# Kernel tuning notes

Hardware: AMD Instinct MI355X
Metric: run time of the kernel (lower is better)

The kernel has to match this reference:

```python
import jax, jax.numpy as jnp
import numpy as np

B, S, D = 4, 2048, 256
H, RANK, DFF = 8, 8, 1024
DK = D // H
EPS = 1e-5


def _linear(x, W, b):
    # torch nn.Linear: y = x @ W.T + b, W shape (out, in)
    return jnp.einsum('bsd,od->bso', x, W) + b


def _layer_norm(x, g, b):
    mu = jnp.mean(x, axis=-1, keepdims=True)
    var = jnp.var(x, axis=-1, keepdims=True)
    return (x - mu) * jax.lax.rsqrt(var + EPS) * g + b


def setup_inputs() -> dict:
    key = jax.random.key(0)
    ks = jax.random.split(key, 20)
    r = RANK * H
    s = lambda fan_in: 1.0 / np.sqrt(fan_in)
    inp = {
        'x': jax.random.normal(ks[0], (B, S, D), jnp.float32),
        'Wq_down': jax.random.uniform(ks[1], (r, D), jnp.float32, -s(D), s(D)),
        'bq_down': jnp.zeros((r,), jnp.float32),
        'Wq_up': jax.random.uniform(ks[2], (D, r), jnp.float32, -s(r), s(r)),
        'bq_up': jnp.zeros((D,), jnp.float32),
        'Wk_down': jax.random.uniform(ks[3], (r, D), jnp.float32, -s(D), s(D)),
        'bk_down': jnp.zeros((r,), jnp.float32),
        'Wk_up': jax.random.uniform(ks[4], (D, r), jnp.float32, -s(r), s(r)),
        'bk_up': jnp.zeros((D,), jnp.float32),
        'Wv': jax.random.uniform(ks[5], (D, D), jnp.float32, -s(D), s(D)),
        'bv': jnp.zeros((D,), jnp.float32),
        'Wo': jax.random.uniform(ks[6], (D, D), jnp.float32, -s(D), s(D)),
        'bo': jnp.zeros((D,), jnp.float32),
        'ln_attn_g': jnp.ones((D,), jnp.float32),
        'ln_attn_b': jnp.zeros((D,), jnp.float32),
        'W_ff1': jax.random.uniform(ks[7], (DFF, D), jnp.float32, -s(D), s(D)),
        'b_ff1': jnp.zeros((DFF,), jnp.float32),
        'W_ff2': jax.random.uniform(ks[8], (D, DFF), jnp.float32, -s(DFF), s(DFF)),
        'b_ff2': jnp.zeros((D,), jnp.float32),
        'ln_blk_g': jnp.ones((D,), jnp.float32),
        'ln_blk_b': jnp.zeros((D,), jnp.float32),
    }
    return inp


def reference(x, Wq_down, bq_down, Wq_up, bq_up, Wk_down, bk_down, Wk_up, bk_up,
              Wv, bv, Wo, bo, ln_attn_g, ln_attn_b,
              W_ff1, b_ff1, W_ff2, b_ff2, ln_blk_g, ln_blk_b):
    # Low-rank Q/K: down-project to rank*H then up-project to D
    Q = _linear(_linear(x, Wq_down, bq_down), Wq_up, bq_up)
    K = _linear(_linear(x, Wk_down, bk_down), Wk_up, bk_up)
    V = _linear(x, Wv, bv)
    # (B,S,D) -> (B,H,S,DK)
    Q = Q.reshape(B, S, H, DK).transpose(0, 2, 1, 3)
    K = K.reshape(B, S, H, DK).transpose(0, 2, 1, 3)
    V = V.reshape(B, S, H, DK).transpose(0, 2, 1, 3)
    scale = 1.0 / np.sqrt(DK).astype(np.float32)
    scores = jnp.einsum('bhqd,bhkd->bhqk', Q, K) * scale
    attn = jax.nn.softmax(scores, axis=-1)
    context = jnp.einsum('bhqk,bhkd->bhqd', attn, V)
    context = context.transpose(0, 2, 1, 3).reshape(B, S, D)
    attn_out = _linear(context, Wo, bo)
    attn_out = _layer_norm(x + attn_out, ln_attn_g, ln_attn_b)
    # FFN: Linear -> GELU (exact erf, torch default) -> Linear
    h = jax.nn.gelu(_linear(attn_out, W_ff1, b_ff1), approximate=False)
    ff = _linear(h, W_ff2, b_ff2)
    return _layer_norm(attn_out + ff, ln_blk_g, ln_blk_b)
```

## Files before the change

kernel.cpp:

```cpp
#include <hip/hip_runtime.h>
#include <hip/hip_bf16.h>
#include <math.h>

#define NB 4
#define NS 2048
#define ND 256
#define NH 8
#define NDK 32
#define NDFF 1024
#define NROWS (NB * NS)
#define KC 4
#define KVB 64
#define KTILES (NS / KC / KVB)
#define QVLD 384

using short8 = __attribute__((ext_vector_type(8))) short;
using f32x4  = __attribute__((ext_vector_type(4))) float;

__device__ __forceinline__ unsigned short f2bf(float f) {
  union { float f; unsigned u; } v; v.f = f;
  unsigned r = v.u + 0x7fffu + ((v.u >> 16) & 1u);
  return (unsigned short)(r >> 16);
}
__device__ __forceinline__ float bf2f(unsigned short u) {
  union { unsigned u; float f; } v; v.u = ((unsigned)u) << 16;
  return v.f;
}
__device__ __forceinline__ unsigned cvt_pk_bf16(float lo, float hi) {
  unsigned r;
  asm("v_cvt_pk_bf16_f32 %0, %1, %2" : "=v"(r) : "v"(lo), "v"(hi));
  return r;
}
__device__ __forceinline__ void gl_lds16(const void* g, void* l) {
  __builtin_amdgcn_global_load_lds(
      (const __attribute__((address_space(1))) unsigned int*)g,
      (__attribute__((address_space(3))) unsigned int*)l, 16, 0, 0);
}

__global__ void cvt_batch(const float* s0, const float* s1, const float* s2,
                          const float* s3, const float* s4, const float* s5,
                          const float* s6, const float* s7,
                          unsigned short* d0, unsigned short* d1,
                          unsigned short* d2, unsigned short* d3,
                          unsigned short* d4, unsigned short* d5,
                          unsigned short* d6, unsigned short* d7,
                          int n0, int n1, int n2, int n3, int n4, int n5,
                          int n6, int n7) {
  const float* s; unsigned short* d; int n;
  switch (blockIdx.y) {
    case 0: s = s0; d = d0; n = n0; break;
    case 1: s = s1; d = d1; n = n1; break;
    case 2: s = s2; d = d2; n = n2; break;
    case 3: s = s3; d = d3; n = n3; break;
    case 4: s = s4; d = d4; n = n4; break;
    case 5: s = s5; d = d5; n = n5; break;
    case 6: s = s6; d = d6; n = n6; break;
    default: s = s7; d = d7; n = n7; break;
  }
  for (int i = (blockIdx.x * 256 + threadIdx.x) * 4; i < n; i += 256 * 256 * 4) {
    float4 v = *reinterpret_cast<const float4*>(s + i);
    ushort4 o;
    o.x = f2bf(v.x); o.y = f2bf(v.y); o.z = f2bf(v.z); o.w = f2bf(v.w);
    *reinterpret_cast<ushort4*>(d + i) = o;
  }
}

template <int BM, int BN, int ACT, int OBF, int RES, int DUAL, int AF32,
          int ACOMB>
__global__ __launch_bounds__(256)
void gemm_nt(const void* __restrict__ Araw, int lda,
             const unsigned short* __restrict__ W,
             const float* __restrict__ bias, const float* __restrict__ bias2,
             int bsplit, const float* __restrict__ bias3, int bsplit2,
             const void* __restrict__ resid, void* __restrict__ outp,
             int K, int O,
             const void* A2, const unsigned short* W2,
             const float* biasB, void* outp2,
             const unsigned short* paccp, const float* plp) {
  constexpr int MFW = BM / 32;
  constexpr int NFW = BN / 32;
  __shared__ __align__(16) unsigned short lA[2][BM * 64];
  __shared__ __align__(16) unsigned short lB[2][BN * 64];
  const int tid = threadIdx.x, lane = tid & 63, wid = tid >> 6;
  const int wr = wid >> 1, wc = wid & 1;
  const int l15 = lane & 15, lg = lane >> 4;
  const int bm = blockIdx.x, bn = blockIdx.y;

  const void* Ap = Araw;
  const unsigned short* Wp = W;
  const float* biasp = bias;
  void* outpp = outp;
  if (DUAL && blockIdx.z) { Ap = A2; Wp = W2; biasp = biasB; outpp = outp2; }

  auto stage = [&](int k0, int buf) {
#pragma unroll
    for (int it = 0; it < BM / 32; ++it) {
      int c = it * 256 + tid;
      int row = c >> 3, cc = (c & 7) ^ (row & 7);
      if (ACOMB) {
        int g = k0 + cc * 8;
        int grow = bm * BM + row;
        int b = grow >> 11, q = grow & 2047;
        int h = g >> 5, d = g & 31;
        size_t base = ((size_t)(b * 8 + h) * 2048 + q) * 32 + d;
        size_t lbase = (size_t)(b * 8 + h) * 2048 + q;
        float o0 = 0, o1 = 0, o2 = 0, o3 = 0, o4 = 0, o5 = 0, o6 = 0, o7 = 0;
        float L = 0.0f;
#pragma unroll
        for (int c2 = 0; c2 < KC; ++c2) {
          short8 a8 = *reinterpret_cast<const short8*>(
              paccp + (size_t)c2 * 2097152 + base);
          o0 += bf2f((unsigned short)a8[0]);
          o1 += bf2f((unsigned short)a8[1]);
          o2 += bf2f((unsigned short)a8[2]);
          o3 += bf2f((unsigned short)a8[3]);
          o4 += bf2f((unsigned short)a8[4]);
          o5 += bf2f((unsigned short)a8[5]);
          o6 += bf2f((unsigned short)a8[6]);
          o7 += bf2f((unsigned short)a8[7]);
          L += plp[(size_t)c2 * 65536 + lbase];
        }
        float inv = 1.0f / L;
        uint4 w;
        w.x = cvt_pk_bf16(o0 * inv, o1 * inv);
        w.y = cvt_pk_bf16(o2 * inv, o3 * inv);
        w.z = cvt_pk_bf16(o4 * inv, o5 * inv);
        w.w = cvt_pk_bf16(o6 * inv, o7 * inv);
        *reinterpret_cast<uint4*>(&lA[buf][c * 8]) = w;
      } else if (AF32) {
        const float* src =
            (const float*)Ap + (size_t)(bm * BM + row) * lda + k0 + cc * 8;
        float4 v0 = *reinterpret_cast<const float4*>(src);
        float4 v1 = *reinterpret_cast<const float4*>(src + 4);
        uint4 w;
        w.x = cvt_pk_bf16(v0.x, v0.y);
        w.y = cvt_pk_bf16(v0.z, v0.w);
        w.z = cvt_pk_bf16(v1.x, v1.y);
        w.w = cvt_pk_bf16(v1.z, v1.w);
        *reinterpret_cast<uint4*>(&lA[buf][c * 8]) = w;
      } else {
        gl_lds16((const unsigned short*)Ap +
                     (size_t)(bm * BM + row) * lda + k0 + cc * 8,
                 &lA[buf][c * 8]);
      }
    }
#pragma unroll
    for (int it = 0; it < BN / 32; ++it) {
      int c = it * 256 + tid;
      int row = c >> 3, cc = (c & 7) ^ (row & 7);
      gl_lds16(Wp + (size_t)(bn * BN + row) * K + k0 + cc * 8, &lB[buf][c * 8]);
    }
  };

  f32x4 acc[MFW][NFW];
#pragma unroll
  for (int i = 0; i < MFW; ++i)
#pragma unroll
    for (int j = 0; j < NFW; ++j) acc[i][j] = (f32x4)0.0f;

  const int T = K >> 6;
  stage(0, 0);
  __syncthreads();
  for (int t = 0; t < T; ++t) {
    const int cur = t & 1;
    if (t + 1 < T) stage((t + 1) << 6, cur ^ 1);
#pragma unroll
    for (int kk = 0; kk < 2; ++kk) {
      short8 a[MFW], b[NFW];
#pragma unroll
      for (int mf = 0; mf < MFW; ++mf) {
        int row = wr * (BM / 2) + mf * 16 + l15;
        a[mf] = *reinterpret_cast<const short8*>(
            &lA[cur][row * 64 + (((kk * 4 + lg) ^ (l15 & 7)) << 3)]);
      }
#pragma unroll
      for (int nf = 0; nf < NFW; ++nf) {
        int row = wc * (BN / 2) + nf * 16 + l15;
        b[nf] = *reinterpret_cast<const short8*>(
            &lB[cur][row * 64 + (((kk * 4 + lg) ^ (l15 & 7)) << 3)]);
      }
#pragma unroll
      for (int mf = 0; mf < MFW; ++mf)
#pragma unroll
        for (int nf = 0; nf < NFW; ++nf)
          acc[mf][nf] = __builtin_amdgcn_mfma_f32_16x16x32_bf16(
              a[mf], b[nf], acc[mf][nf], 0, 0, 0);
    }
    __syncthreads();
  }

#pragma unroll
  for (int mf = 0; mf < MFW; ++mf)
#pragma unroll
    for (int nf = 0; nf < NFW; ++nf) {
      int col = bn * BN + wc * (BN / 2) + nf * 16 + l15;
      float bv;
      if (bias3 && col >= bsplit2) bv = bias3[col - bsplit2];
      else if (bias2 && col >= bsplit) bv = bias2[col - bsplit];
      else bv = biasp[col];
#pragma unroll
      for (int i = 0; i < 4; ++i) {
        int row = bm * BM + wr * (BM / 2) + mf * 16 + lg * 4 + i;
        float v = acc[mf][nf][i] + bv;
        if (ACT == 1) v = 0.5f * v * (1.0f + erff(v * 0.70710678118654752f));
        if (RES == 1)
          v += ((const float*)resid)[(size_t)row * O + col];
        else if (RES == 2)
          v += bf2f(((const unsigned short*)resid)[(size_t)row * O + col]);
        if (OBF)
          ((unsigned short*)outpp)[(size_t)row * O + col] = f2bf(v);
        else
          ((float*)outpp)[(size_t)row * O + col] = v;
      }
    }
}

__global__ __launch_bounds__(256)
void attn_kernel(const unsigned short* __restrict__ Qb,
                 const unsigned short* __restrict__ Kb,
                 const unsigned short* __restrict__ qv,
                 unsigned short* __restrict__ pacc,
                 float* __restrict__ pl) {
  __shared__ __align__(16) unsigned short lK[2][KVB * 32];
  __shared__ __align__(16) unsigned short lVt[2][32 * 64];
  __shared__ __align__(16) unsigned short lP[4][16 * 64];
  const int tid = threadIdx.x, lane = tid & 63, wid = tid >> 6;
  const int l15 = lane & 15, lg = lane >> 4;
  const int bh = blockIdx.x, qt = blockIdx.y, kc = blockIdx.z;
  const int b = bh >> 3, h = bh & 7;
  const size_t headoff = (size_t)h * NDK;
  const int qbase = qt * 128 + wid * 32;
  const int kv0 = kc * (NS / KC);
  const float qscale = 0.25508686f;

  short8 aq[2];
#pragma unroll
  for (int r = 0; r < 2; ++r) {
    short8 v = *reinterpret_cast<const short8*>(
        Qb + (size_t)(b * NS + qbase + r * 16 + l15) * ND + headoff + lg * 8);
#pragma unroll
    for (int j = 0; j < 8; ++j)
      v[j] = (short)f2bf(bf2f((unsigned short)v[j]) * qscale);
    aq[r] = v;
  }

  const unsigned short* kptr =
      Kb + (size_t)(b * NS + kv0 + (tid >> 2)) * ND + headoff +
      (((tid & 3) ^ ((tid >> 3) & 3)) << 3);
  const int vd0 = (tid & 15) * 2, vb = tid >> 4;
  const unsigned short* vptr =
      qv + (size_t)(b * NS + kv0 + vb * 4) * QVLD + 128 + headoff + vd0;
  const int vbs = vb ^ ((((tid & 15) * 2 >> 1) & 7) << 1);

  auto writeV = [&](const unsigned* w, int buf) {
    unsigned lo0 = (w[0] & 0xffffu) | (w[1] << 16);
    unsigned lo1 = (w[2] & 0xffffu) | (w[3] << 16);
    unsigned hi0 = (w[0] >> 16) | (w[1] & 0xffff0000u);
    unsigned hi1 = (w[2] >> 16) | (w[3] & 0xffff0000u);
    *reinterpret_cast<uint2*>(&lVt[buf][vd0 * 64 + vbs * 4]) =
        make_uint2(lo0, lo1);
    *reinterpret_cast<uint2*>(&lVt[buf][(vd0 + 1) * 64 + vbs * 4]) =
        make_uint2(hi0, hi1);
  };

  f32x4 accT[2][2];
#pragma unroll
  for (int r = 0; r < 2; ++r)
#pragma unroll
    for (int d = 0; d < 2; ++d) accT[r][d] = (f32x4)0.0f;
  float l[2] = {0.0f, 0.0f};

  unsigned vr[4];
  gl_lds16(kptr, &lK[0][tid * 8]);
#pragma unroll
  for (int u = 0; u < 4; ++u)
    vr[u] = *reinterpret_cast<const unsigned*>(vptr + (size_t)u * QVLD);
  writeV(vr, 0);
  __syncthreads();

  for (int kt = 0; kt < KTILES; ++kt) {
    const int cur = kt & 1, nxt = cur ^ 1;
    const bool pf = (kt + 1 < KTILES);
    if (pf) {
      kptr += (size_t)KVB * ND;
      vptr += (size_t)KVB * QVLD;
      gl_lds16(kptr, &lK[nxt][tid * 8]);
#pragma unroll
      for (int u = 0; u < 4; ++u)
        vr[u] = *reinterpret_cast<const unsigned*>(vptr + (size_t)u * QVLD);
    }

#pragma unroll
    for (int r = 0; r < 2; ++r) {
      f32x4 sT[4];
      __builtin_amdgcn_s_setprio(1);
#pragma unroll
      for (int t = 0; t < 4; ++t) {
        short8 bk = *reinterpret_cast<const short8*>(
            &lK[cur][(t * 16 + l15) * 32 + ((lg ^ ((l15 >> 1) & 3)) << 3)]);
        sT[t] = __builtin_amdgcn_mfma_f32_16x16x32_bf16(
            bk, aq[r], (f32x4)0.0f, 0, 0, 0);
      }
      __builtin_amdgcn_s_setprio(0);
#pragma unroll
      for (int t = 0; t < 4; ++t) {
        float p0 = __builtin_amdgcn_exp2f(sT[t][0]);
        float p1 = __builtin_amdgcn_exp2f(sT[t][1]);
        float p2 = __builtin_amdgcn_exp2f(sT[t][2]);
        float p3 = __builtin_amdgcn_exp2f(sT[t][3]);
        l[r] += (p0 + p1) + (p2 + p3);
        unsigned w0 = cvt_pk_bf16(p0, p1);
        unsigned w1 = cvt_pk_bf16(p2, p3);
        int blk = (t << 1) | (lg >> 1);
        *reinterpret_cast<uint2*>(
            &lP[wid][l15 * 64 + ((blk ^ (l15 & 7)) << 3) + ((lg & 1) << 2)]) =
            make_uint2(w0, w1);
      }
      __builtin_amdgcn_s_setprio(1);
#pragma unroll
      for (int kk = 0; kk < 2; ++kk) {
        short8 pa = *reinterpret_cast<const short8*>(
            &lP[wid][l15 * 64 + (((kk * 4 + lg) ^ (l15 & 7)) << 3)]);
#pragma unroll
        for (int dt = 0; dt < 2; ++dt) {
          int row = dt * 16 + l15;
          int bb = ((kk * 4 + lg) << 1) ^ (((l15 >> 1) & 7) << 1);
          short8 bv = *reinterpret_cast<const short8*>(
              &lVt[cur][row * 64 + (bb << 2)]);
          accT[r][dt] = __builtin_amdgcn_mfma_f32_16x16x32_bf16(
              bv, pa, accT[r][dt], 0, 0, 0);
        }
      }
      __builtin_amdgcn_s_setprio(0);
    }

    if (pf) writeV(vr, nxt);
    __syncthreads();
  }

#pragma unroll
  for (int r = 0; r < 2; ++r) {
    l[r] += __shfl_xor(l[r], 16);
    l[r] += __shfl_xor(l[r], 32);
  }

#pragma unroll
  for (int r = 0; r < 2; ++r) {
    int qg = qbase + r * 16 + l15;
    size_t rowbase = ((size_t)kc * 65536 + (size_t)bh * NS + qg) * 32;
#pragma unroll
    for (int dt = 0; dt < 2; ++dt) {
      unsigned w0 = cvt_pk_bf16(accT[r][dt][0], accT[r][dt][1]);
      unsigned w1 = cvt_pk_bf16(accT[r][dt][2], accT[r][dt][3]);
      *reinterpret_cast<uint2*>(&pacc[rowbase + dt * 16 + lg * 4]) =
          make_uint2(w0, w1);
    }
  }
  if (lane < 16) {
#pragma unroll
    for (int r = 0; r < 2; ++r) {
      int qg = qbase + r * 16 + l15;
      pl[(size_t)kc * 65536 + (size_t)bh * NS + qg] = l[r];
    }
  }
}

__global__ __launch_bounds__(256)
void ln_res_kernel(const float* __restrict__ a,
                   const float* __restrict__ g, const float* __restrict__ be,
                   float* yf, unsigned short* yb) {
  int row = blockIdx.x * 4 + (threadIdx.x >> 6);
  int lane = threadIdx.x & 63;
  size_t off = (size_t)row * ND + lane * 4;
  float4 va = *reinterpret_cast<const float4*>(a + off);
  float v0 = va.x, v1 = va.y, v2 = va.z, v3 = va.w;
  float s = v0 + v1 + v2 + v3;
  float sq = v0 * v0 + v1 * v1 + v2 * v2 + v3 * v3;
#pragma unroll
  for (int o = 1; o < 64; o <<= 1) {
    s += __shfl_xor(s, o);
    sq += __shfl_xor(sq, o);
  }
  float mu = s * (1.0f / 256.0f);
  float var = sq * (1.0f / 256.0f) - mu * mu;
  float rs = rsqrtf(var + 1e-5f);
  float4 vg = *reinterpret_cast<const float4*>(g + lane * 4);
  float4 vbe = *reinterpret_cast<const float4*>(be + lane * 4);
  float o0 = (v0 - mu) * rs * vg.x + vbe.x;
  float o1 = (v1 - mu) * rs * vg.y + vbe.y;
  float o2 = (v2 - mu) * rs * vg.z + vbe.z;
  float o3 = (v3 - mu) * rs * vg.w + vbe.w;
  if (yf) *reinterpret_cast<float4*>(yf + off) = make_float4(o0, o1, o2, o3);
  if (yb) {
    ushort4 ob;
    ob.x = f2bf(o0); ob.y = f2bf(o1); ob.z = f2bf(o2); ob.w = f2bf(o3);
    *reinterpret_cast<ushort4*>(yb + off) = ob;
  }
}

extern "C" void kernel_launch(void* const* d_in, const int* in_sizes, int n_in,
                              void* d_out, int out_size, void* d_ws,
                              size_t ws_size, hipStream_t stream) {
  (void)in_sizes; (void)n_in; (void)out_size; (void)ws_size;
  const float* x   = (const float*)d_in[0];
  const float* Wqd = (const float*)d_in[1];
  const float* bqd = (const float*)d_in[2];
  const float* Wqu = (const float*)d_in[3];
  const float* bqu = (const float*)d_in[4];
  const float* Wkd = (const float*)d_in[5];
  const float* bkd = (const float*)d_in[6];
  const float* Wku = (const float*)d_in[7];
  const float* bku = (const float*)d_in[8];
  const float* Wv  = (const float*)d_in[9];
  const float* bv  = (const float*)d_in[10];
  const float* Wo  = (const float*)d_in[11];
  const float* bo  = (const float*)d_in[12];
  const float* g1  = (const float*)d_in[13];
  const float* be1 = (const float*)d_in[14];
  const float* Wf1 = (const float*)d_in[15];
  const float* bf1 = (const float*)d_in[16];
  const float* Wf2 = (const float*)d_in[17];
  const float* bf2 = (const float*)d_in[18];
  const float* g2  = (const float*)d_in[19];
  const float* be2 = (const float*)d_in[20];

  char* p = (char*)d_ws;
  auto alloc = [&](size_t bytes) {
    char* r = p;
    p += (bytes + 255) & ~(size_t)255;
    return r;
  };
  unsigned short* wqkv = (unsigned short*)alloc(384 * 256 * 2);
  unsigned short* wqu  = (unsigned short*)alloc(256 * 64 * 2);
  unsigned short* wku  = (unsigned short*)alloc(256 * 64 * 2);
  unsigned short* wo   = (unsigned short*)alloc(256 * 256 * 2);
  unsigned short* wf1  = (unsigned short*)alloc(1024 * 256 * 2);
  unsigned short* wf2  = (unsigned short*)alloc(256 * 1024 * 2);
  unsigned short* qv   = (unsigned short*)alloc((size_t)NROWS * QVLD * 2);
  unsigned short* Qb   = (unsigned short*)alloc((size_t)NROWS * ND * 2);
  unsigned short* Kb   = (unsigned short*)alloc((size_t)NROWS * ND * 2);
  float*          pl   = (float*)alloc((size_t)KC * 65536 * 4);
  unsigned short* y1b  = (unsigned short*)alloc((size_t)NROWS * ND * 2);
  unsigned short* hb   = (unsigned short*)alloc((size_t)NROWS * NDFF * 2);
  float* ao = (float*)d_out;

  unsigned short* pacc = hb;

  cvt_batch<<<dim3(256, 8), 256, 0, stream>>>(
      Wqd, Wkd, Wqu, Wku, Wv, Wo, Wf1, Wf2,
      wqkv, wqkv + 64 * 256, wqu, wku, wqkv + 128 * 256, wo, wf1, wf2,
      64 * 256, 64 * 256, 256 * 64, 256 * 64, 256 * 256,
      256 * 256, 1024 * 256, 256 * 1024);

  gemm_nt<64, 64, 0, 1, 0, 0, 1, 0><<<dim3(128, 6), 256, 0, stream>>>(
      x, 256, wqkv, bqd, bkd, 64, bv, 128, nullptr, qv, 256, QVLD,
      nullptr, nullptr, nullptr, nullptr, nullptr, nullptr);
  gemm_nt<64, 64, 0, 1, 0, 1, 0, 0><<<dim3(128, 4, 2), 256, 0, stream>>>(
      qv, QVLD, wqu, bqu, nullptr, 0, nullptr, 0, nullptr, Qb, 64, 256,
      qv + 64, wku, bku, Kb, nullptr, nullptr);

  attn_kernel<<<dim3(NB * NH, NS / 128, KC), 256, 0, stream>>>(
      Qb, Kb, qv, pacc, pl);

  gemm_nt<64, 64, 0, 0, 1, 0, 0, 1><<<dim3(128, 4), 256, 0, stream>>>(
      nullptr, 256, wo, bo, nullptr, 0, nullptr, 0, x, ao, 256, 256,
      nullptr, nullptr, nullptr, nullptr, pacc, pl);
  ln_res_kernel<<<NROWS / 4, 256, 0, stream>>>(ao, g1, be1, nullptr, y1b);

  gemm_nt<128, 128, 1, 1, 0, 0, 0, 0><<<dim3(64, 8), 256, 0, stream>>>(
      y1b, 256, wf1, bf1, nullptr, 0, nullptr, 0, nullptr, hb, 256, NDFF,
      nullptr, nullptr, nullptr, nullptr, nullptr, nullptr);
  gemm_nt<64, 64, 0, 0, 2, 0, 0, 0><<<dim3(128, 4), 256, 0, stream>>>(
      hb, 1024, wf2, bf2, nullptr, 0, nullptr, 0, y1b, ao, 1024, 256,
      nullptr, nullptr, nullptr, nullptr, nullptr, nullptr);
  ln_res_kernel<<<NROWS / 4, 256, 0, stream>>>(ao, g2, be2,
                                               (float*)d_out, nullptr);
}
```

Before: 106.7 us.

## Split-K the FFN2 GEMM across two halves and move softmax row sums onto MFMA

The second FFN GEMM (K=1024) now runs as a two-way split-K using the dual-z mode: each half covers 512 of K into a separate fp32 buffer, and the final layernorm sums the two partials. This doubles the grid of that GEMM, which had only 512 blocks, at the cost of an extra fp32 buffer write and read. In the attention kernel, the per-row softmax denominator is now computed with an MFMA against a vector of bf16 ones instead of scalar adds and cross-lane shuffles. That sum is taken from the bf16-rounded probabilities, so it matches the numerator more closely.

After: 107.1 us. No clear change (+0.3%).

```diff
diff --git a/kernel.cpp b/kernel.cpp
--- a/kernel.cpp
+++ b/kernel.cpp
@@ -69,7 +69,7 @@
           int ACOMB>
 __global__ __launch_bounds__(256)
 void gemm_nt(const void* __restrict__ Araw, int lda,
-             const unsigned short* __restrict__ W,
+             const unsigned short* __restrict__ W, int ldw,
              const float* __restrict__ bias, const float* __restrict__ bias2,
              int bsplit, const float* __restrict__ bias3, int bsplit2,
              const void* __restrict__ resid, void* __restrict__ outp,
@@ -90,7 +90,10 @@
   const unsigned short* Wp = W;
   const float* biasp = bias;
   void* outpp = outp;
-  if (DUAL && blockIdx.z) { Ap = A2; Wp = W2; biasp = biasB; outpp = outp2; }
+  if (DUAL && blockIdx.z) {
+    Ap = A2; Wp = W2; outpp = outp2;
+    if (DUAL == 1) biasp = biasB;
+  }
 
   auto stage = [&](int k0, int buf) {
 #pragma unroll
@@ -148,7 +151,8 @@
     for (int it = 0; it < BN / 32; ++it) {
       int c = it * 256 + tid;
       int row = c >> 3, cc = (c & 7) ^ (row & 7);
-      gl_lds16(Wp + (size_t)(bn * BN + row) * K + k0 + cc * 8, &lB[buf][c * 8]);
+      gl_lds16(Wp + (size_t)(bn * BN + row) * ldw + k0 + cc * 8,
+               &lB[buf][c * 8]);
     }
   };
 
@@ -189,13 +193,15 @@
     __syncthreads();
   }
 
+  const bool zhalf = (DUAL == 2) && blockIdx.z;
 #pragma unroll
   for (int mf = 0; mf < MFW; ++mf)
 #pragma unroll
     for (int nf = 0; nf < NFW; ++nf) {
       int col = bn * BN + wc * (BN / 2) + nf * 16 + l15;
       float bv;
-      if (bias3 && col >= bsplit2) bv = bias3[col - bsplit2];
+      if (zhalf) bv = 0.0f;
+      else if (bias3 && col >= bsplit2) bv = bias3[col - bsplit2];
       else if (bias2 && col >= bsplit) bv = bias2[col - bsplit];
       else bv = biasp[col];
 #pragma unroll
@@ -203,9 +209,9 @@
         int row = bm * BM + wr * (BM / 2) + mf * 16 + lg * 4 + i;
         float v = acc[mf][nf][i] + bv;
         if (ACT == 1) v = 0.5f * v * (1.0f + erff(v * 0.70710678118654752f));
-        if (RES == 1)
+        if (RES == 1 && !zhalf)
           v += ((const float*)resid)[(size_t)row * O + col];
-        else if (RES == 2)
+        else if (RES == 2 && !zhalf)
           v += bf2f(((const unsigned short*)resid)[(size_t)row * O + col]);
         if (OBF)
           ((unsigned short*)outpp)[(size_t)row * O + col] = f2bf(v);
@@ -243,6 +249,9 @@
       v[j] = (short)f2bf(bf2f((unsigned short)v[j]) * qscale);
     aq[r] = v;
   }
+  short8 ones8;
+#pragma unroll
+  for (int j = 0; j < 8; ++j) ones8[j] = (short)0x3F80;
 
   const unsigned short* kptr =
       Kb + (size_t)(b * NS + kv0 + (tid >> 2)) * ND + headoff +
@@ -264,11 +273,13 @@
   };
 
   f32x4 accT[2][2];
-#pragma unroll
-  for (int r = 0; r < 2; ++r)
+  f32x4 accL[2];
+#pragma unroll
+  for (int r = 0; r < 2; ++r) {
+    accL[r] = (f32x4)0.0f;
 #pragma unroll
     for (int d = 0; d < 2; ++d) accT[r][d] = (f32x4)0.0f;
-  float l[2] = {0.0f, 0.0f};
+  }
 
   unsigned vr[4];
   gl_lds16(kptr, &lK[0][tid * 8]);
@@ -308,7 +319,6 @@
         float p1 = __builtin_amdgcn_exp2f(sT[t][1]);
         float p2 = __builtin_amdgcn_exp2f(sT[t][2]);
         float p3 = __builtin_amdgcn_exp2f(sT[t][3]);
-        l[r] += (p0 + p1) + (p2 + p3);
         unsigned w0 = cvt_pk_bf16(p0, p1);
         unsigned w1 = cvt_pk_bf16(p2, p3);
         int blk = (t << 1) | (lg >> 1);
@@ -321,6 +331,8 @@
       for (int kk = 0; kk < 2; ++kk) {
         short8 pa = *reinterpret_cast<const short8*>(
             &lP[wid][l15 * 64 + (((kk * 4 + lg) ^ (l15 & 7)) << 3)]);
+        accL[r] = __builtin_amdgcn_mfma_f32_16x16x32_bf16(
+            ones8, pa, accL[r], 0, 0, 0);
 #pragma unroll
         for (int dt = 0; dt < 2; ++dt) {
           int row = dt * 16 + l15;
@@ -340,12 +352,6 @@
 
 #pragma unroll
   for (int r = 0; r < 2; ++r) {
-    l[r] += __shfl_xor(l[r], 16);
-    l[r] += __shfl_xor(l[r], 32);
-  }
-
-#pragma unroll
-  for (int r = 0; r < 2; ++r) {
     int qg = qbase + r * 16 + l15;
     size_t rowbase = ((size_t)kc * 65536 + (size_t)bh * NS + qg) * 32;
 #pragma unroll
@@ -360,13 +366,13 @@
 #pragma unroll
     for (int r = 0; r < 2; ++r) {
       int qg = qbase + r * 16 + l15;
-      pl[(size_t)kc * 65536 + (size_t)bh * NS + qg] = l[r];
+      pl[(size_t)kc * 65536 + (size_t)bh * NS + qg] = accL[r][0];
     }
   }
 }
 
 __global__ __launch_bounds__(256)
-void ln_res_kernel(const float* __restrict__ a,
+void ln_res_kernel(const float* __restrict__ a, const float* bsrc,
                    const float* __restrict__ g, const float* __restrict__ be,
                    float* yf, unsigned short* yb) {
   int row = blockIdx.x * 4 + (threadIdx.x >> 6);
@@ -374,6 +380,10 @@
   size_t off = (size_t)row * ND + lane * 4;
   float4 va = *reinterpret_cast<const float4*>(a + off);
   float v0 = va.x, v1 = va.y, v2 = va.z, v3 = va.w;
+  if (bsrc) {
+    float4 vb = *reinterpret_cast<const float4*>(bsrc + off);
+    v0 += vb.x; v1 += vb.y; v2 += vb.z; v3 += vb.w;
+  }
   float s = v0 + v1 + v2 + v3;
   float sq = v0 * v0 + v1 * v1 + v2 * v2 + v3 * v3;
 #pragma unroll
@@ -441,6 +451,7 @@
   unsigned short* Kb   = (unsigned short*)alloc((size_t)NROWS * ND * 2);
   float*          pl   = (float*)alloc((size_t)KC * 65536 * 4);
   unsigned short* y1b  = (unsigned short*)alloc((size_t)NROWS * ND * 2);
+  float*          ao2  = (float*)alloc((size_t)NROWS * ND * 4);
   unsigned short* hb   = (unsigned short*)alloc((size_t)NROWS * NDFF * 2);
   float* ao = (float*)d_out;
 
@@ -453,26 +464,27 @@
       256 * 256, 1024 * 256, 256 * 1024);
 
   gemm_nt<64, 64, 0, 1, 0, 0, 1, 0><<<dim3(128, 6), 256, 0, stream>>>(
-      x, 256, wqkv, bqd, bkd, 64, bv, 128, nullptr, qv, 256, QVLD,
+      x, 256, wqkv, 256, bqd, bkd, 64, bv, 128, nullptr, qv, 256, QVLD,
       nullptr, nullptr, nullptr, nullptr, nullptr, nullptr);
   gemm_nt<64, 64, 0, 1, 0, 1, 0, 0><<<dim3(128, 4, 2), 256, 0, stream>>>(
-      qv, QVLD, wqu, bqu, nullptr, 0, nullptr, 0, nullptr, Qb, 64, 256,
+      qv, QVLD, wqu, 64, bqu, nullptr, 0, nullptr, 0, nullptr, Qb, 64, 256,
       qv + 64, wku, bku, Kb, nullptr, nullptr);
 
   attn_kernel<<<dim3(NB * NH, NS / 128, KC), 256, 0, stream>>>(
       Qb, Kb, qv, pacc, pl);
 
   gemm_nt<64, 64, 0, 0, 1, 0, 0, 1><<<dim3(128, 4), 256, 0, stream>>>(
-      nullptr, 256, wo, bo, nullptr, 0, nullptr, 0, x, ao, 256, 256,
+      nullptr, 256, wo, 256, bo, nullptr, 0, nullptr, 0, x, ao, 256, 256,
       nullptr, nullptr, nullptr, nullptr, pacc, pl);
-  ln_res_kernel<<<NROWS / 4, 256, 0, stream>>>(ao, g1, be1, nullptr, y1b);
+  ln_res_kernel<<<NROWS / 4, 256, 0, stream>>>(ao, nullptr, g1, be1,
+                                               nullptr, y1b);
 
   gemm_nt<128, 128, 1, 1, 0, 0, 0, 0><<<dim3(64, 8), 256, 0, stream>>>(
-      y1b, 256, wf1, bf1, nullptr, 0, nullptr, 0, nullptr, hb, 256, NDFF,
+      y1b, 256, wf1, 256, bf1, nullptr, 0, nullptr, 0, nullptr, hb, 256, NDFF,
       nullptr, nullptr, nullptr, nullptr, nullptr, nullptr);
-  gemm_nt<64, 64, 0, 0, 2, 0, 0, 0><<<dim3(128, 4), 256, 0, stream>>>(
-      hb, 1024, wf2, bf2, nullptr, 0, nullptr, 0, y1b, ao, 1024, 256,
-      nullptr, nullptr, nullptr, nullptr, nullptr, nullptr);
-  ln_res_kernel<<<NROWS / 4, 256, 0, stream>>>(ao, g2, be2,
+  gemm_nt<64, 64, 0, 0, 2, 2, 0, 0><<<dim3(128, 4, 2), 256, 0, stream>>>(
+      hb, 1024, wf2, 1024, bf2, nullptr, 0, nullptr, 0, y1b, ao, 512, 256,
+      hb + 512, wf2 + 512, nullptr, ao2, nullptr, nullptr);
+  ln_res_kernel<<<NROWS / 4, 256, 0, stream>>>(ao, ao2, g2, be2,
                                                (float*)d_out, nullptr);
 }
```
